# Performance work log

Hardware: AMD Instinct MI355X
Metric: run time of the kernel (lower is better)

The kernel has to match this reference:

```python
import jax, jax.numpy as jnp
import numpy as np

NEG_INF = -1e30


def setup_inputs() -> dict:
    key = jax.random.key(0)
    ks = jax.random.split(key, 11)
    b, n, d = 4, 2048, 1024
    scale = 1.0 / np.sqrt(d)
    inp = {
        "q": jax.random.normal(ks[0], (b, n, d), jnp.float32),
        "k": jax.random.normal(ks[1], (b, n, d), jnp.float32),
        "v": jax.random.normal(ks[2], (b, n, d), jnp.float32),
        # nn.Linear params: weight [out, in], bias [out]
        "Wq": jax.random.normal(ks[3], (d, d), jnp.float32) * scale,
        "bq": jnp.zeros((d,), jnp.float32),
        "Wk": jax.random.normal(ks[4], (d, d), jnp.float32) * scale,
        "bk": jnp.zeros((d,), jnp.float32),
        "Wv": jax.random.normal(ks[5], (d, d), jnp.float32) * scale,
        "bv": jnp.zeros((d,), jnp.float32),
        "Wo": jax.random.normal(ks[6], (d, d), jnp.float32) * scale,
        "bo": jnp.zeros((d,), jnp.float32),
    }
    return inp


def reference(q, k, v, Wq, bq, Wk, bk, Wv, bv, Wo, bo):
    # Faithful to source: the multi-head reshape/transpose results are never
    # assigned, so attention runs single-headed over full n_embd vectors.
    b, n, d = q.shape
    qp = q @ Wq.T + bq  # [b, n, d]
    kp = k @ Wk.T + bk
    vp = v @ Wv.T + bv
    scale = jnp.asarray(1.0 / d, qp.dtype) ** 0.5  # sqrt(1/d)
    att = jnp.einsum('bnd,bmd->bnm', qp, kp) * scale  # [b, n, n]
    causal = jnp.tril(jnp.ones((n, n), bool))          # block_size tril sliced to n
    att = jnp.where(causal[None, :, :], att, NEG_INF)
    att = jax.nn.softmax(att, axis=-1)  # dropout p=0.0 -> identity
    y = att @ vp                        # [b, n, d]
    # source bug reproduced: transpose(1,2) then reshape(b, n, d)
    y = jnp.swapaxes(y, 1, 2).reshape(b, n, d)
    y = y @ Wo.T + bo
    return y
```

## Files before the change

kernel.cpp:

```cpp
#include <hip/hip_runtime.h>
#include <hip/hip_bf16.h>
#include <stdint.h>

typedef __bf16 bf16_t;
typedef __bf16 bf16x8 __attribute__((ext_vector_type(8)));
typedef __bf16 bf16x4 __attribute__((ext_vector_type(4)));
typedef float f32x4 __attribute__((ext_vector_type(4)));

#define GLD_LDS16(src, dst)                                                              \
  __builtin_amdgcn_global_load_lds((const __attribute__((address_space(1))) void*)(src), \
                                   (__attribute__((address_space(3))) void*)(dst), 16, 0, 0)

#define BAR() __builtin_amdgcn_s_barrier()
#define LGKM0() asm volatile("s_waitcnt lgkmcnt(0)" ::: "memory")
#define VMC6() asm volatile("s_waitcnt vmcnt(6)" ::: "memory")
#define VMC0() asm volatile("s_waitcnt vmcnt(0)" ::: "memory")

__device__ __forceinline__ int swz(int x) { return x ^ (((x >> 9) & 1) << 5); }

struct CvtArgs {
  const float* src[7];
  bf16_t* dst[7];
  long n4[7];
};

__global__ __launch_bounds__(256) void cvt_all(CvtArgs a) {
  const int seg = blockIdx.y;
  const float* __restrict__ in = a.src[seg];
  bf16_t* __restrict__ out = a.dst[seg];
  const long n4 = a.n4[seg];
  long i = (long)blockIdx.x * blockDim.x + threadIdx.x;
  const long stride = (long)gridDim.x * blockDim.x;
  for (; i < n4; i += stride) {
    float4 v = ((const float4*)in)[i];
    bf16x4 o;
    o[0] = (bf16_t)v.x; o[1] = (bf16_t)v.y; o[2] = (bf16_t)v.z; o[3] = (bf16_t)v.w;
    ((bf16x4*)out)[i] = o;
  }
}

__global__ __launch_bounds__(256) void softmax_causal(bf16_t* __restrict__ S, int n, long sB) {
  const int i = blockIdx.x;
  const int z = blockIdx.y;
  bf16_t* row = S + (long)z * sB + (long)i * n;
  const int t = threadIdx.x;
  const int j0 = t << 3;

  bf16x8 vv = ((const bf16x8*)row)[t];
  float vals[8];
  float mx = -3.0e38f;
#pragma unroll
  for (int e = 0; e < 8; ++e) {
    float v = (j0 + e <= i) ? (float)vv[e] : -3.0e38f;
    vals[e] = v;
    mx = fmaxf(mx, v);
  }
#pragma unroll
  for (int off = 32; off; off >>= 1) mx = fmaxf(mx, __shfl_xor(mx, off));
  __shared__ float redm[4];
  if ((t & 63) == 0) redm[t >> 6] = mx;
  __syncthreads();
  mx = fmaxf(fmaxf(redm[0], redm[1]), fmaxf(redm[2], redm[3]));

  float sum = 0.f;
#pragma unroll
  for (int e = 0; e < 8; ++e) {
    float p = (j0 + e <= i) ? __expf(vals[e] - mx) : 0.f;
    vals[e] = p;
    sum += p;
  }
#pragma unroll
  for (int off = 32; off; off >>= 1) sum += __shfl_xor(sum, off);
  __shared__ float reds[4];
  if ((t & 63) == 0) reds[t >> 6] = sum;
  __syncthreads();
  sum = reds[0] + reds[1] + reds[2] + reds[3];
  const float inv = 1.0f / sum;

  bf16x8 o;
#pragma unroll
  for (int e = 0; e < 8; ++e) o[e] = (bf16_t)(vals[e] * inv);
  ((bf16x8*)row)[t] = o;
}

__device__ __forceinline__ void xcd_remap(int& bx, int& by, int& bz) {
  const int gx = gridDim.x, gy = gridDim.y;
  int lin = (blockIdx.z * gy + blockIdx.y) * gx + blockIdx.x;
  const int nwg = gx * gy * (int)gridDim.z;
  lin = (lin & 7) * (nwg >> 3) + (lin >> 3);
  bx = lin % gx;
  const int rem = lin / gx;
  by = rem % gy;
  bz = rem / gy;
}

struct G8Args {
  const bf16_t* A[3];
  const bf16_t* W[3];
  const float* bias[3];
  bf16_t* C[3];
  long sA, sB, sC;
};

template <int HALF, int BUF>
__device__ __forceinline__ void stage8(char* lds, const bf16_t* srcH, const int (&soff)[2],
                                       int wid, int tile) {
  const bf16_t* s = srcH + tile * 64;
  char* d = lds + (HALF >= 2 ? 65536 : 0) + BUF * 32768 + (HALF & 1) * 16384 + wid * 2048;
  GLD_LDS16(s + soff[0], d);
  GLD_LDS16(s + soff[1], d + 1024);
}

template <int BUF, int QM>
__device__ __forceinline__ void rdA(char* lds, const int (&aoffp)[4][2], bf16x8 (&af)[4][2]) {
  char* b = lds + BUF * 32768 + QM * 16384;
#pragma unroll
  for (int mi = 0; mi < 4; ++mi)
#pragma unroll
    for (int kk = 0; kk < 2; ++kk) af[mi][kk] = *(const bf16x8*)(b + aoffp[mi][kk]);
}

template <int BUF, int QN>
__device__ __forceinline__ void rdB(char* lds, const int (&boffp)[2][2], bf16x8 (&bf)[2][2]) {
  char* b = lds + 65536 + BUF * 32768 + QN * 16384;
#pragma unroll
  for (int ni = 0; ni < 2; ++ni)
#pragma unroll
    for (int kk = 0; kk < 2; ++kk) bf[ni][kk] = *(const bf16x8*)(b + boffp[ni][kk]);
}

template <int QM, int QN>
__device__ __forceinline__ void mm16(f32x4 (&acc)[2][2][4][2], const bf16x8 (&af)[4][2],
                                     const bf16x8 (&bf)[2][2]) {
  __builtin_amdgcn_s_setprio(1);
#pragma unroll
  for (int mi = 0; mi < 4; ++mi)
#pragma unroll
    for (int ni = 0; ni < 2; ++ni)
#pragma unroll
      for (int kk = 0; kk < 2; ++kk)
        acc[QM][QN][mi][ni] = __builtin_amdgcn_mfma_f32_16x16x32_bf16(
            af[mi][kk], bf[ni][kk], acc[QM][QN][mi][ni], 0, 0, 0);
  __builtin_amdgcn_s_setprio(0);
}

template <int MODE>
__global__ __launch_bounds__(512, 2) void gemm8(G8Args ga) {
  int bx, by, bz;
  xcd_remap(bx, by, bz);
  const int m0 = by << 8, n0 = bx << 8;
  if (MODE == 1 && n0 > m0 + 255) return;

  const int K = 1024, NT = 16;
  const bf16_t* A;
  const bf16_t* B;
  const float* bias = nullptr;
  if (MODE == 0) {
    A = ga.A[bz]; B = ga.W[bz]; bias = ga.bias[bz];
  } else {
    A = ga.A[0] + (long)bz * ga.sA;
    B = ga.W[0] + (long)bz * ga.sB;
  }

  __shared__ __align__(16) char lds[131072];

  const int t = threadIdx.x;
  const int wid = t >> 6, l = t & 63;
  const int wm = wid >> 2, wn = wid & 3;
  const int ri16 = l & 15, kg = l >> 4;

  int soff[2];
#pragma unroll
  for (int i = 0; i < 2; ++i) {
    const int sub = wid * 2 + i;
    const int ri = l >> 2;
    const int cq = (l & 3) ^ ((ri & 8) >> 2);
    const int r = (sub >> 1) * 16 + ri;
    const int c = (sub & 1) * 32 + cq * 8;
    soff[i] = r * K + c;
  }
  const bf16_t* srcA0 = A + (long)m0 * K;
  const bf16_t* srcA1 = A + (long)(m0 + 128) * K;
  const bf16_t* srcB0 = B + (long)n0 * K;
  const bf16_t* srcB1 = B + (long)(n0 + 128) * K;

  int aoffp[4][2], boffp[2][2];
#pragma unroll
  for (int mi = 0; mi < 4; ++mi)
#pragma unroll
    for (int kk = 0; kk < 2; ++kk)
      aoffp[mi][kk] = swz((wm * 4 + mi) * 2048 + kk * 1024 + ri16 * 64 + kg * 16);
#pragma unroll
  for (int ni = 0; ni < 2; ++ni)
#pragma unroll
    for (int kk = 0; kk < 2; ++kk)
      boffp[ni][kk] = swz((wn * 2 + ni) * 2048 + kk * 1024 + ri16 * 64 + kg * 16);

  f32x4 acc[2][2][4][2] = {};
  bf16x8 af[4][2], bf0[2][2], bf1[2][2];

  stage8<0, 0>(lds, srcA0, soff, wid, 0);
  stage8<2, 0>(lds, srcB0, soff, wid, 0);
  stage8<3, 0>(lds, srcB1, soff, wid, 0);
  stage8<1, 0>(lds, srcA1, soff, wid, 0);
  stage8<0, 1>(lds, srcA0, soff, wid, 1);
  stage8<2, 1>(lds, srcB0, soff, wid, 1);
  stage8<3, 1>(lds, srcB1, soff, wid, 1);
  VMC6();
  BAR();

  for (int tt = 0; tt < NT; tt += 2) {
    const bool hasNext = (tt + 2) < NT;
    rdA<0, 0>(lds, aoffp, af);
    rdB<0, 0>(lds, boffp, bf0);
    stage8<1, 1>(lds, srcA1, soff, wid, tt + 1);
    BAR(); LGKM0();
    mm16<0, 0>(acc, af, bf0);
    BAR();
    rdB<0, 1>(lds, boffp, bf1);
    if (hasNext) stage8<0, 0>(lds, srcA0, soff, wid, tt + 2);
    BAR(); LGKM0();
    mm16<0, 1>(acc, af, bf1);
    BAR();
    rdA<0, 1>(lds, aoffp, af);
    if (hasNext) stage8<2, 0>(lds, srcB0, soff, wid, tt + 2);
    BAR(); LGKM0();
    mm16<1, 0>(acc, af, bf0);
    BAR();
    if (hasNext) stage8<3, 0>(lds, srcB1, soff, wid, tt + 2);
    BAR(); LGKM0();
    mm16<1, 1>(acc, af, bf1);
    if (hasNext) { VMC6(); } else { VMC0(); }
    BAR();
    rdA<1, 0>(lds, aoffp, af);
    rdB<1, 0>(lds, boffp, bf0);
    if (hasNext) stage8<1, 0>(lds, srcA1, soff, wid, tt + 2);
    BAR(); LGKM0();
    mm16<0, 0>(acc, af, bf0);
    BAR();
    rdB<1, 1>(lds, boffp, bf1);
    if (hasNext) stage8<0, 1>(lds, srcA0, soff, wid, tt + 3);
    BAR(); LGKM0();
    mm16<0, 1>(acc, af, bf1);
    BAR();
    rdA<1, 1>(lds, aoffp, af);
    if (hasNext) stage8<2, 1>(lds, srcB0, soff, wid, tt + 3);
    BAR(); LGKM0();
    mm16<1, 0>(acc, af, bf0);
    BAR();
    if (hasNext) stage8<3, 1>(lds, srcB1, soff, wid, tt + 3);
    BAR(); LGKM0();
    mm16<1, 1>(acc, af, bf1);
    if (hasNext) { VMC6(); }
    BAR();
  }

  if (MODE == 0) {
    if (bz < 2) {
      bf16_t* C = ga.C[bz];
#pragma unroll
      for (int qm = 0; qm < 2; ++qm)
#pragma unroll
        for (int qn = 0; qn < 2; ++qn)
#pragma unroll
          for (int mi = 0; mi < 4; ++mi)
#pragma unroll
            for (int ni = 0; ni < 2; ++ni) {
              const int col = n0 + qn * 128 + wn * 32 + ni * 16 + ri16;
              const int row0 = m0 + qm * 128 + wm * 64 + mi * 16 + kg * 4;
              const float badd = bias[col];
#pragma unroll
              for (int j = 0; j < 4; ++j)
                C[(long)(row0 + j) * 1024 + col] = (bf16_t)(acc[qm][qn][mi][ni][j] + badd);
            }
    } else {
      bf16_t* C = ga.C[2];
#pragma unroll
      for (int qm = 0; qm < 2; ++qm)
#pragma unroll
        for (int qn = 0; qn < 2; ++qn)
#pragma unroll
          for (int mi = 0; mi < 4; ++mi)
#pragma unroll
            for (int ni = 0; ni < 2; ++ni) {
              const int col = n0 + qn * 128 + wn * 32 + ni * 16 + ri16;
              const int row0 = m0 + qm * 128 + wm * 64 + mi * 16 + kg * 4;
              const float badd = bias[col];
              const int batch = row0 >> 11, nr = row0 & 2047;
              bf16x4 o;
#pragma unroll
              for (int j = 0; j < 4; ++j) o[j] = (bf16_t)(acc[qm][qn][mi][ni][j] + badd);
              *(bf16x4*)(C + (long)batch * (2048 * 1024) + (long)col * 2048 + nr) = o;
            }
    }
  } else {
    bf16_t* C = ga.C[0] + (long)bz * ga.sC;
#pragma unroll
    for (int qm = 0; qm < 2; ++qm)
#pragma unroll
      for (int qn = 0; qn < 2; ++qn)
#pragma unroll
        for (int mi = 0; mi < 4; ++mi)
#pragma unroll
          for (int ni = 0; ni < 2; ++ni) {
            const int col = n0 + qn * 128 + wn * 32 + ni * 16 + ri16;
            const int row0 = m0 + qm * 128 + wm * 64 + mi * 16 + kg * 4;
#pragma unroll
            for (int j = 0; j < 4; ++j)
              C[(long)(row0 + j) * 2048 + col] = (bf16_t)(acc[qm][qn][mi][ni][j] * 0.03125f);
          }
  }
}

template <bool BF16_OUT, bool BIAS, bool KBOUND>
__device__ __forceinline__ void gemm_body(const bf16_t* __restrict__ A,
                                          const bf16_t* __restrict__ B,
                                          const float* __restrict__ bias,
                                          void* __restrict__ Cout,
                                          int N, int K, float alpha,
                                          int m0, int n0) {
  int KT = K >> 5;
  if (KBOUND) {
    int kb = (n0 + 128) >> 5;
    if (kb < KT) KT = kb;
  }

  __shared__ __align__(16) bf16_t As[128 * 32];
  __shared__ __align__(16) bf16_t Bs[128 * 32];

  const int t = threadIdx.x;
  const int l = t & 63;
  const int w = t >> 6;
  const int wr = w >> 1, wc = w & 1;

  const int c0 = t, c1 = t + 256;
  const bf16_t* a_src0 = A + (long)(m0 + (c0 >> 2)) * K + ((c0 & 3) << 3);
  const bf16_t* a_src1 = A + (long)(m0 + (c1 >> 2)) * K + ((c1 & 3) << 3);
  const bf16_t* b_src0 = B + (long)(n0 + (c0 >> 2)) * K + ((c0 & 3) << 3);
  const bf16_t* b_src1 = B + (long)(n0 + (c1 >> 2)) * K + ((c1 & 3) << 3);
  char* const asb = (char*)As;
  char* const bsb = (char*)Bs;
  char* const a_dst0 = asb + w * 1024;
  char* const a_dst1 = asb + 4096 + w * 1024;
  char* const b_dst0 = bsb + w * 1024;
  char* const b_dst1 = bsb + 4096 + w * 1024;

  const int r16 = l & 15, kg = l >> 4;
  int aoff[4], boff[4];
#pragma unroll
  for (int mi = 0; mi < 4; ++mi) aoff[mi] = (((wr * 64 + mi * 16 + r16) * 32) + kg * 8) * 2;
#pragma unroll
  for (int ni = 0; ni < 4; ++ni) boff[ni] = (((wc * 64 + ni * 16 + r16) * 32) + kg * 8) * 2;

  f32x4 acc[4][4] = {};

  for (int kt = 0; kt < KT; ++kt) {
    __syncthreads();
    GLD_LDS16(a_src0, a_dst0);
    GLD_LDS16(a_src1, a_dst1);
    GLD_LDS16(b_src0, b_dst0);
    GLD_LDS16(b_src1, b_dst1);
    a_src0 += 32; a_src1 += 32; b_src0 += 32; b_src1 += 32;
    __syncthreads();

    bf16x8 af[4], bfr[4];
#pragma unroll
    for (int mi = 0; mi < 4; ++mi) af[mi] = *(const bf16x8*)(asb + aoff[mi]);
#pragma unroll
    for (int ni = 0; ni < 4; ++ni) bfr[ni] = *(const bf16x8*)(bsb + boff[ni]);
#pragma unroll
    for (int mi = 0; mi < 4; ++mi)
#pragma unroll
      for (int ni = 0; ni < 4; ++ni)
        acc[mi][ni] = __builtin_amdgcn_mfma_f32_16x16x32_bf16(af[mi], bfr[ni], acc[mi][ni], 0, 0, 0);
  }

  const int rowbase = m0 + wr * 64 + ((l >> 4) << 2);
  const int colbase = n0 + wc * 64 + (l & 15);
  if constexpr (BF16_OUT) {
    bf16_t* C = (bf16_t*)Cout;
#pragma unroll
    for (int mi = 0; mi < 4; ++mi)
#pragma unroll
      for (int ni = 0; ni < 4; ++ni) {
        const int col = colbase + ni * 16;
        float badd = 0.f;
        if constexpr (BIAS) badd = bias[col];
#pragma unroll
        for (int j = 0; j < 4; ++j) {
          float v = acc[mi][ni][j] * alpha + badd;
          C[(long)(rowbase + mi * 16 + j) * N + col] = (bf16_t)v;
        }
      }
  } else {
    float* C = (float*)Cout;
#pragma unroll
    for (int mi = 0; mi < 4; ++mi)
#pragma unroll
      for (int ni = 0; ni < 4; ++ni) {
        const int col = colbase + ni * 16;
        float badd = 0.f;
        if constexpr (BIAS) badd = bias[col];
#pragma unroll
        for (int j = 0; j < 4; ++j) {
          float v = acc[mi][ni][j] * alpha + badd;
          C[(long)(rowbase + mi * 16 + j) * N + col] = v;
        }
      }
  }
}

template <bool BF16_OUT, bool BIAS, bool KBOUND>
__global__ __launch_bounds__(256, 4) void gemm_bt(const bf16_t* __restrict__ A,
                                                  const bf16_t* __restrict__ B,
                                                  const float* __restrict__ bias,
                                                  void* __restrict__ Cout,
                                                  int N, int K, float alpha,
                                                  long sAb, long sBb, long sCb, int eltC) {
  int bx, by, bz;
  xcd_remap(bx, by, bz);
  const int m0 = by << 7, n0 = bx << 7;
  gemm_body<BF16_OUT, BIAS, KBOUND>(A + (long)bz * sAb, B + (long)bz * sBb, bias,
                                    (char*)Cout + (long)bz * sCb * eltC, N, K, alpha, m0, n0);
}

extern "C" void kernel_launch(void* const* d_in, const int* in_sizes, int n_in,
                              void* d_out, int out_size, void* d_ws, size_t ws_size,
                              hipStream_t stream) {
  const int b = 4, n = 2048, d = 1024;
  const long nd  = (long)n * d;
  const long bn  = (long)b * n;
  const long bnd = bn * d;
  const long ddl = (long)d * d;
  const long nn  = (long)n * n;

  const float* q  = (const float*)d_in[0];
  const float* k  = (const float*)d_in[1];
  const float* v  = (const float*)d_in[2];
  const float* Wq = (const float*)d_in[3];
  const float* bq = (const float*)d_in[4];
  const float* Wk = (const float*)d_in[5];
  const float* bk = (const float*)d_in[6];
  const float* Wv = (const float*)d_in[7];
  const float* bv = (const float*)d_in[8];
  const float* Wo = (const float*)d_in[9];
  const float* bo = (const float*)d_in[10];

  bf16_t* ws  = (bf16_t*)d_ws;
  bf16_t* qB  = ws;
  bf16_t* kB  = qB + bnd;
  bf16_t* vB  = kB + bnd;
  bf16_t* WqB = vB + bnd;
  bf16_t* WkB = WqB + ddl;
  bf16_t* WvB = WkB + ddl;
  bf16_t* WoB = WvB + ddl;
  bf16_t* qpB = WoB + ddl;
  bf16_t* kpB = qpB + bnd;
  bf16_t* vpT = kpB + bnd;
  bf16_t* S   = vpT + bnd;
  bf16_t* yT  = S + (long)b * nn;
  const size_t need = (size_t)(7 * bnd + 4 * ddl + (long)b * nn) * 2;
  if (ws_size < need) return;

  dim3 blk(256);

  CvtArgs ca;
  ca.src[0] = q;  ca.dst[0] = qB;  ca.n4[0] = bnd / 4;
  ca.src[1] = k;  ca.dst[1] = kB;  ca.n4[1] = bnd / 4;
  ca.src[2] = v;  ca.dst[2] = vB;  ca.n4[2] = bnd / 4;
  ca.src[3] = Wq; ca.dst[3] = WqB; ca.n4[3] = ddl / 4;
  ca.src[4] = Wk; ca.dst[4] = WkB; ca.n4[4] = ddl / 4;
  ca.src[5] = Wv; ca.dst[5] = WvB; ca.n4[5] = ddl / 4;
  ca.src[6] = Wo; ca.dst[6] = WoB; ca.n4[6] = ddl / 4;
  cvt_all<<<dim3(512, 7), blk, 0, stream>>>(ca);

  G8Args qa = {};
  qa.A[0] = qB; qa.W[0] = WqB; qa.bias[0] = bq; qa.C[0] = qpB;
  qa.A[1] = kB; qa.W[1] = WkB; qa.bias[1] = bk; qa.C[1] = kpB;
  qa.A[2] = vB; qa.W[2] = WvB; qa.bias[2] = bv; qa.C[2] = vpT;
  gemm8<0><<<dim3(d / 256, bn / 256, 3), dim3(512), 0, stream>>>(qa);

  G8Args sa = {};
  sa.A[0] = qpB; sa.W[0] = kpB; sa.C[0] = S;
  sa.sA = nd; sa.sB = nd; sa.sC = nn;
  gemm8<1><<<dim3(n / 256, n / 256, b), dim3(512), 0, stream>>>(sa);

  softmax_causal<<<dim3(n, b), blk, 0, stream>>>(S, n, nn);

  gemm_bt<true, false, true><<<dim3(n / 128, d / 128, b), blk, 0, stream>>>(
      vpT, S, nullptr, yT, n, n, 1.f, nd, nn, nd, 2);

  gemm_bt<false, true, false><<<dim3(d / 128, bn / 128, 1), blk, 0, stream>>>(
      yT, WoB, bo, (float*)d_out, d, d, 1.f, 0, 0, 0, 4);
}
```

Baseline: 220.9 us.

## Software-pipeline LDS fragment reads with MFMA in 8-wave GEMM main loop

Restructures the GEMM K-loop so each phase issues the MFMA block on already-loaded fragments while reading the next fragments from LDS and staging global loads, using one barrier per phase instead of two. Scheduling barriers pin the instruction order, and vmcnt waits are retuned to match the new order of outstanding loads. The last iteration is peeled into a template variant. This aims to hide LDS read latency behind matrix instructions and halve barrier count. It risks LDS hazards if the wait counts or the reuse of buffers are wrong.

Result: faster. 210.7 us (-4.6%).

```diff
diff --git a/kernel.cpp b/kernel.cpp
--- a/kernel.cpp
+++ b/kernel.cpp
@@ -13,8 +13,8 @@
 
 #define BAR() __builtin_amdgcn_s_barrier()
 #define LGKM0() asm volatile("s_waitcnt lgkmcnt(0)" ::: "memory")
-#define VMC6() asm volatile("s_waitcnt vmcnt(6)" ::: "memory")
-#define VMC0() asm volatile("s_waitcnt vmcnt(0)" ::: "memory")
+#define VMCN(n) asm volatile("s_waitcnt vmcnt(" #n ")" ::: "memory")
+#define SCH0() __builtin_amdgcn_sched_barrier(0)
 
 __device__ __forceinline__ int swz(int x) { return x ^ (((x >> 9) & 1) << 5); }
 
@@ -144,6 +144,59 @@
   __builtin_amdgcn_s_setprio(0);
 }
 
+template <bool LAST>
+__device__ __forceinline__ void kiter(char* lds, int tt,
+    const bf16_t* srcA0, const bf16_t* srcA1, const bf16_t* srcB0, const bf16_t* srcB1,
+    const int (&soff)[2], int wid,
+    const int (&aoffp)[4][2], const int (&boffp)[2][2],
+    bf16x8 (&af)[4][2], bf16x8 (&bf0)[2][2], bf16x8 (&bf1)[2][2],
+    f32x4 (&acc)[2][2][4][2]) {
+  VMCN(8); LGKM0(); SCH0();
+  mm16<0, 0>(acc, af, bf0);
+  rdB<0, 1>(lds, boffp, bf1);
+  stage8<1, 1>(lds, srcA1, soff, wid, tt + 1);
+  SCH0(); BAR();
+  VMCN(8); LGKM0(); SCH0();
+  mm16<0, 1>(acc, af, bf1);
+  rdA<0, 1>(lds, aoffp, af);
+  if (!LAST) stage8<0, 0>(lds, srcA0, soff, wid, tt + 2);
+  SCH0(); BAR();
+  if (LAST) { VMCN(0); } else { VMCN(6); }
+  LGKM0(); SCH0();
+  mm16<1, 0>(acc, af, bf0);
+  rdB<1, 0>(lds, boffp, bf0);
+  if (!LAST) stage8<2, 0>(lds, srcB0, soff, wid, tt + 2);
+  SCH0(); BAR();
+  LGKM0(); SCH0();
+  mm16<1, 1>(acc, af, bf1);
+  rdA<1, 0>(lds, aoffp, af);
+  if (!LAST) stage8<3, 0>(lds, srcB1, soff, wid, tt + 2);
+  SCH0(); BAR();
+  if (!LAST) { VMCN(8); }
+  LGKM0(); SCH0();
+  mm16<0, 0>(acc, af, bf0);
+  rdB<1, 1>(lds, boffp, bf1);
+  if (!LAST) stage8<1, 0>(lds, srcA1, soff, wid, tt + 2);
+  SCH0(); BAR();
+  if (!LAST) { VMCN(8); }
+  LGKM0(); SCH0();
+  mm16<0, 1>(acc, af, bf1);
+  rdA<1, 1>(lds, aoffp, af);
+  if (!LAST) stage8<0, 1>(lds, srcA0, soff, wid, tt + 3);
+  SCH0(); BAR();
+  if (!LAST) { VMCN(6); }
+  LGKM0(); SCH0();
+  mm16<1, 0>(acc, af, bf0);
+  if (!LAST) rdB<0, 0>(lds, boffp, bf0);
+  if (!LAST) stage8<2, 1>(lds, srcB0, soff, wid, tt + 3);
+  SCH0(); BAR();
+  LGKM0(); SCH0();
+  mm16<1, 1>(acc, af, bf1);
+  if (!LAST) rdA<0, 0>(lds, aoffp, af);
+  if (!LAST) stage8<3, 1>(lds, srcB1, soff, wid, tt + 3);
+  SCH0(); BAR();
+}
+
 template <int MODE>
 __global__ __launch_bounds__(512, 2) void gemm8(G8Args ga) {
   int bx, by, bz;
@@ -206,54 +259,16 @@
   stage8<0, 1>(lds, srcA0, soff, wid, 1);
   stage8<2, 1>(lds, srcB0, soff, wid, 1);
   stage8<3, 1>(lds, srcB1, soff, wid, 1);
-  VMC6();
+  VMCN(6);
   BAR();
-
-  for (int tt = 0; tt < NT; tt += 2) {
-    const bool hasNext = (tt + 2) < NT;
-    rdA<0, 0>(lds, aoffp, af);
-    rdB<0, 0>(lds, boffp, bf0);
-    stage8<1, 1>(lds, srcA1, soff, wid, tt + 1);
-    BAR(); LGKM0();
-    mm16<0, 0>(acc, af, bf0);
-    BAR();
-    rdB<0, 1>(lds, boffp, bf1);
-    if (hasNext) stage8<0, 0>(lds, srcA0, soff, wid, tt + 2);
-    BAR(); LGKM0();
-    mm16<0, 1>(acc, af, bf1);
-    BAR();
-    rdA<0, 1>(lds, aoffp, af);
-    if (hasNext) stage8<2, 0>(lds, srcB0, soff, wid, tt + 2);
-    BAR(); LGKM0();
-    mm16<1, 0>(acc, af, bf0);
-    BAR();
-    if (hasNext) stage8<3, 0>(lds, srcB1, soff, wid, tt + 2);
-    BAR(); LGKM0();
-    mm16<1, 1>(acc, af, bf1);
-    if (hasNext) { VMC6(); } else { VMC0(); }
-    BAR();
-    rdA<1, 0>(lds, aoffp, af);
-    rdB<1, 0>(lds, boffp, bf0);
-    if (hasNext) stage8<1, 0>(lds, srcA1, soff, wid, tt + 2);
-    BAR(); LGKM0();
-    mm16<0, 0>(acc, af, bf0);
-    BAR();
-    rdB<1, 1>(lds, boffp, bf1);
-    if (hasNext) stage8<0, 1>(lds, srcA0, soff, wid, tt + 3);
-    BAR(); LGKM0();
-    mm16<0, 1>(acc, af, bf1);
-    BAR();
-    rdA<1, 1>(lds, aoffp, af);
-    if (hasNext) stage8<2, 1>(lds, srcB0, soff, wid, tt + 3);
-    BAR(); LGKM0();
-    mm16<1, 0>(acc, af, bf0);
-    BAR();
-    if (hasNext) stage8<3, 1>(lds, srcB1, soff, wid, tt + 3);
-    BAR(); LGKM0();
-    mm16<1, 1>(acc, af, bf1);
-    if (hasNext) { VMC6(); }
-    BAR();
-  }
+  rdA<0, 0>(lds, aoffp, af);
+  rdB<0, 0>(lds, boffp, bf0);
+
+  for (int tt = 0; tt + 2 < NT; tt += 2)
+    kiter<false>(lds, tt, srcA0, srcA1, srcB0, srcB1, soff, wid, aoffp, boffp,
+                 af, bf0, bf1, acc);
+  kiter<true>(lds, NT - 2, srcA0, srcA1, srcB0, srcB1, soff, wid, aoffp, boffp,
+              af, bf0, bf1, acc);
 
   if (MODE == 0) {
     if (bz < 2) {
```
